# Performance work log

Measured on AMD Instinct MI355X. Metric: run time of the kernel, lower is better.

The kernel has to match this reference:

```python
import jax, jax.numpy as jnp
import numpy as np

N = 50000   # nodes
E = 800000  # directed edges
IN = 128
H = 128


def setup_inputs() -> dict:
    key = jax.random.key(0)
    k1, k2, k3, k4 = jax.random.split(key, 4)
    x = jax.random.normal(k1, (N, IN), jnp.float32)
    edge_index = jax.random.randint(k2, (2, E), 0, N, jnp.int32)
    W1 = jax.random.normal(k3, (IN, H), jnp.float32) / np.sqrt(IN)
    b1 = jnp.zeros((H,), jnp.float32)
    W2 = jax.random.normal(k4, (H, H), jnp.float32) / np.sqrt(H)
    b2 = jnp.zeros((H,), jnp.float32)
    return {"x": x, "edge_index": edge_index, "W1": W1, "b1": b1, "W2": W2, "b2": b2}


def _gcn_norm(edge_index, num_nodes):
    # PyG GCNConv default: add self-loops, symmetric normalization D^-1/2 A D^-1/2
    row, col = edge_index[0], edge_index[1]
    loop = jnp.arange(num_nodes, dtype=row.dtype)
    row = jnp.concatenate([row, loop])
    col = jnp.concatenate([col, loop])
    deg = jax.ops.segment_sum(jnp.ones_like(row, jnp.float32), row, num_segments=num_nodes)
    dinv = jnp.where(deg > 0, jax.lax.rsqrt(deg), 0.0)
    norm = dinv[row] * dinv[col]  # [E + N]
    return row, col, norm


def _gcn_conv(x, W, b, row, col, norm, num_nodes):
    xw = x @ W                                  # [N, H] dense GEMM
    msg = norm[:, None] * xw[col]               # gather + scale, [E+N, H]
    out = jax.ops.segment_sum(msg, row, num_segments=num_nodes)  # scatter-add
    return out + b


def reference(x, edge_index, W1, b1, W2, b2):
    row, col, norm = _gcn_norm(edge_index, N)
    h = _gcn_conv(x, W1, b1, row, col, norm, N)
    h = jax.nn.relu(h)
    out = _gcn_conv(h, W2, b2, row, col, norm, N)
    return out
```

## Files before the change

kernel.cpp:

```cpp
#include <hip/hip_runtime.h>

#define NN 50000
#define NE 800000
#define HD 128
#define NBK 98
#define BCAP 16384
#define FB 196
#define CVB 200

using short8 = __attribute__((ext_vector_type(8))) short;
using f32x4  = __attribute__((ext_vector_type(4))) float;

__device__ inline unsigned short rne_bf16(float v) {
    union { float f; unsigned u; } c; c.f = v;
    return (unsigned short)((c.u + 0x7fff + ((c.u >> 16) & 1)) >> 16);
}
__device__ inline float bf16_to_f32(unsigned short h) {
    union { unsigned u; float f; } c; c.u = ((unsigned)h) << 16;
    return c.f;
}


__global__ __launch_bounds__(256) void k_fill1(const int* __restrict__ ei,
                                               int* __restrict__ bcur,
                                               int2* __restrict__ pairs,
                                               const float* __restrict__ W1,
                                               const float* __restrict__ W2,
                                               unsigned short* __restrict__ hi1,
                                               unsigned short* __restrict__ lo1,
                                               unsigned short* __restrict__ hi2,
                                               unsigned short* __restrict__ lo2,
                                               const float* __restrict__ x,
                                               unsigned short* __restrict__ xb) {
    int t = threadIdx.x, b = blockIdx.x;
    if (b >= FB + 16) {
        int bb = b - (FB + 16);
        const int total = NN * HD / 8;
        for (int i = bb * 256 + t; i < total; i += CVB * 256) {
            float4 a0 = ((const float4*)x)[i * 2];
            float4 a1 = ((const float4*)x)[i * 2 + 1];
            short8 r;
            r[0] = (short)rne_bf16(a0.x); r[1] = (short)rne_bf16(a0.y);
            r[2] = (short)rne_bf16(a0.z); r[3] = (short)rne_bf16(a0.w);
            r[4] = (short)rne_bf16(a1.x); r[5] = (short)rne_bf16(a1.y);
            r[6] = (short)rne_bf16(a1.z); r[7] = (short)rne_bf16(a1.w);
            *(short8*)(xb + (size_t)i * 8) = r;
        }
        return;
    }
    if (b >= FB) {
        int bb = b - FB;
        const float* W = (bb < 8) ? W1 : W2;
        unsigned short* hi = (bb < 8) ? hi1 : hi2;
        unsigned short* lo = (bb < 8) ? lo1 : lo2;
        int tid = (bb & 7) * 256 + t;
        int lane = tid & 63;
        int ks = (tid >> 6) & 3;
        int nt = tid >> 8;
        int n = nt * 16 + (lane & 15);
        int k0 = ks * 32 + (lane >> 4) * 8;
#pragma unroll
        for (int j = 0; j < 8; ++j) {
            float v = W[(k0 + j) * HD + n];
            unsigned short h = rne_bf16(v);
            float rem = v - bf16_to_f32(h);
            hi[(size_t)tid * 8 + j] = h;
            lo[(size_t)tid * 8 + j] = rne_bf16(rem);
        }
        return;
    }
    __shared__ int dr[4096], sc[4096];
    __shared__ int hist[NBK], base[NBK];
    for (int i = t; i < NBK; i += 256) hist[i] = 0;
    __syncthreads();
    int e0 = b * 4096;
#pragma unroll
    for (int u = 0; u < 16; ++u) {
        int idx = u * 256 + t, e = e0 + idx;
        int r = -1, c = 0;
        if (e < NE) {
            r = ei[e];
            c = ei[NE + e];
            atomicAdd(&hist[r >> 9], 1);
        }
        dr[idx] = r;
        sc[idx] = c;
    }
    __syncthreads();
    for (int i = t; i < NBK; i += 256) {
        base[i] = atomicAdd(&bcur[i], hist[i]);
        hist[i] = 0;
    }
    __syncthreads();
#pragma unroll
    for (int u = 0; u < 16; ++u) {
        int idx = u * 256 + t;
        int r = dr[idx];
        if (r >= 0) {
            int bk = r >> 9;
            int pos = atomicAdd(&hist[bk], 1);
            pairs[(size_t)bk * BCAP + base[bk] + pos] = make_int2(r, sc[idx]);
        }
    }
}


__global__ __launch_bounds__(256) void k_fill2(const int2* __restrict__ pairs,
                                               const int* __restrict__ bcur,
                                               int* __restrict__ deg,
                                               int* __restrict__ offs,
                                               float* __restrict__ dinv,
                                               int* __restrict__ csr) {
    __shared__ int spart[256];
    __shared__ int cnt[512];
    __shared__ int lcur[512];
    int b = blockIdx.x, t = threadIdx.x;
    int n0 = b * 512;
    int nodes = min(512, NN - n0);

    int v = (t < NBK && t < b) ? bcur[t] : 0;
    spart[t] = v;
    __syncthreads();
#pragma unroll
    for (int o = 128; o > 0; o >>= 1) {
        if (t < o) spart[t] += spart[t + o];
        __syncthreads();
    }
    int base = spart[0];
    int tot = bcur[b];

    for (int i = t; i < 512; i += 256) cnt[i] = 0;
    __syncthreads();
    const int2* pp = pairs + (size_t)b * BCAP;
    for (int p = t; p < tot; p += 256) atomicAdd(&cnt[pp[p].x - n0], 1);
    __syncthreads();

    int d0 = (2 * t < nodes) ? cnt[2 * t] : 0;
    int d1 = (2 * t + 1 < nodes) ? cnt[2 * t + 1] : 0;
    spart[t] = d0 + d1;
    __syncthreads();
#pragma unroll
    for (int o = 1; o < 256; o <<= 1) {
        int x = (t >= o) ? spart[t - o] : 0;
        __syncthreads();
        spart[t] += x;
        __syncthreads();
    }
    int excl = spart[t] - (d0 + d1);
    int o0 = base + excl, o1 = o0 + d0;
    if (2 * t < nodes) {
        offs[n0 + 2 * t] = o0;
        lcur[2 * t] = o0;
        deg[n0 + 2 * t] = d0;
        dinv[n0 + 2 * t] = rsqrtf((float)(d0 + 1));
    }
    if (2 * t + 1 < nodes) {
        offs[n0 + 2 * t + 1] = o1;
        lcur[2 * t + 1] = o1;
        deg[n0 + 2 * t + 1] = d1;
        dinv[n0 + 2 * t + 1] = rsqrtf((float)(d1 + 1));
    }
    __syncthreads();

    for (int p = t; p < tot; p += 256) {
        int2 pr = pp[p];
        int slot = atomicAdd(&lcur[pr.x - n0], 1);
        csr[slot] = pr.y;
    }
}


__global__ __launch_bounds__(256) void k_agg_bf16(const unsigned short* __restrict__ src,
                                                  const int* __restrict__ csr,
                                                  const int* __restrict__ offs,
                                                  const int* __restrict__ deg,
                                                  const float* __restrict__ dinv,
                                                  unsigned short* __restrict__ dst) {
    int node = blockIdx.x * 4 + (threadIdx.x >> 6);
    int lane = threadIdx.x & 63;
    int q = lane >> 4;
    int sub = lane & 15;
    int o = offs[node];
    int dg = deg[node];
    float d = dinv[node];

    float acc[8];
    if (q == 0) {
        float s = d * d;
        short8 v = *(const short8*)(src + (size_t)node * HD + sub * 8);
#pragma unroll
        for (int i = 0; i < 8; ++i) acc[i] = s * bf16_to_f32((unsigned short)v[i]);
    } else {
#pragma unroll
        for (int i = 0; i < 8; ++i) acc[i] = 0.0f;
    }

    for (int base = 0; base < dg; base += 64) {
        int n = min(64, dg - base);
        int myc = (lane < n) ? csr[o + base + lane] : node;
        float myw = (lane < n) ? d * dinv[myc] : 0.0f;
        for (int j = 0; j * 4 < n; ++j) {
            int c = __shfl(myc, j * 4 + q);
            float w = __shfl(myw, j * 4 + q);
            short8 v = *(const short8*)(src + (size_t)c * HD + sub * 8);
#pragma unroll
            for (int i = 0; i < 8; ++i)
                acc[i] = fmaf(w, bf16_to_f32((unsigned short)v[i]), acc[i]);
        }
    }

#pragma unroll
    for (int i = 0; i < 8; ++i) {
        acc[i] += __shfl_xor(acc[i], 16);
        acc[i] += __shfl_xor(acc[i], 32);
    }
    if (q == 0) {
        short8 r;
#pragma unroll
        for (int i = 0; i < 8; ++i) r[i] = (short)rne_bf16(acc[i]);
        *(short8*)(dst + (size_t)node * HD + sub * 8) = r;
    }
}


template <bool RELU, bool OUTBF16>
__global__ __launch_bounds__(256) void k_gemm_mfma(const unsigned short* __restrict__ A,
                                                   const unsigned short* __restrict__ Whi,
                                                   const unsigned short* __restrict__ Wlo,
                                                   const float* __restrict__ bias,
                                                   void* __restrict__ Cout, int nrows) {
    int l = threadIdx.x & 63;
    int w = threadIdx.x >> 6;
    int row0 = blockIdx.x * 64 + w * 16;
    int arow = row0 + (l & 15);
    int kj = (l >> 4) * 8;
    bool avalid = (arow < nrows);
    const unsigned short* ap = A + (size_t)(avalid ? arow : 0) * HD + kj;

    f32x4 acc[8];
#pragma unroll
    for (int nt = 0; nt < 8; ++nt) acc[nt] = (f32x4){0.f, 0.f, 0.f, 0.f};

#pragma unroll
    for (int ks = 0; ks < 4; ++ks) {
        short8 ahi = {0, 0, 0, 0, 0, 0, 0, 0};
        if (avalid) ahi = *(const short8*)(ap + ks * 32);
#pragma unroll
        for (int nt = 0; nt < 8; ++nt) {
            size_t fo = ((size_t)(nt * 4 + ks) * 64 + l) * 8;
            short8 bhi = *(const short8*)(Whi + fo);
            short8 blo = *(const short8*)(Wlo + fo);
            acc[nt] = __builtin_amdgcn_mfma_f32_16x16x32_bf16(ahi, bhi, acc[nt], 0, 0, 0);
            acc[nt] = __builtin_amdgcn_mfma_f32_16x16x32_bf16(ahi, blo, acc[nt], 0, 0, 0);
        }
    }

#pragma unroll
    for (int nt = 0; nt < 8; ++nt) {
        int col = nt * 16 + (l & 15);
        float bv = bias[col];
#pragma unroll
        for (int r = 0; r < 4; ++r) {
            int gr = row0 + (l >> 4) * 4 + r;
            if (gr >= nrows) continue;
            float v = acc[nt][r] + bv;
            if (RELU) v = fmaxf(v, 0.f);
            if (OUTBF16)
                ((unsigned short*)Cout)[(size_t)gr * HD + col] = rne_bf16(v);
            else
                ((float*)Cout)[(size_t)gr * HD + col] = v;
        }
    }
}


extern "C" void kernel_launch(void* const* d_in, const int* in_sizes, int n_in,
                              void* d_out, int out_size, void* d_ws, size_t ws_size,
                              hipStream_t stream) {
    const float* x  = (const float*)d_in[0];
    const int*   ei = (const int*)d_in[1];
    const float* W1 = (const float*)d_in[2];
    const float* b1 = (const float*)d_in[3];
    const float* W2 = (const float*)d_in[4];
    const float* b2 = (const float*)d_in[5];
    float* out = (float*)d_out;

    char* ws = (char*)d_ws;
    size_t off = 0;
    auto alloc = [&](size_t bytes) {
        void* p = ws + off;
        off = (off + bytes + 255) & ~(size_t)255;
        return p;
    };
    int*   bcur = (int*)alloc(NBK * 4);
    int*   deg  = (int*)alloc(NN * 4);
    int*   offs = (int*)alloc(NN * 4);
    float* dinv = (float*)alloc(NN * 4);
    int*   csr  = (int*)alloc((size_t)NE * 4);
    unsigned short* xb  = (unsigned short*)alloc((size_t)NN * HD * 2);
    unsigned short* t1b = (unsigned short*)alloc((size_t)NN * HD * 2);
    char* region = (char*)alloc((size_t)NBK * BCAP * 8);
    int2* pairs = (int2*)region;
    unsigned short* hb = (unsigned short*)region;
    unsigned short* Whi1 = (unsigned short*)alloc(16384 * 2);
    unsigned short* Wlo1 = (unsigned short*)alloc(16384 * 2);
    unsigned short* Whi2 = (unsigned short*)alloc(16384 * 2);
    unsigned short* Wlo2 = (unsigned short*)alloc(16384 * 2);

    hipMemsetAsync(bcur, 0, NBK * 4, stream);
    k_fill1<<<FB + 16 + CVB, 256, 0, stream>>>(ei, bcur, pairs, W1, W2,
                                               Whi1, Wlo1, Whi2, Wlo2, x, xb);
    k_fill2<<<NBK, 256, 0, stream>>>(pairs, bcur, deg, offs, dinv, csr);

    k_agg_bf16<<<NN / 4, 256, 0, stream>>>(xb, csr, offs, deg, dinv, t1b);
    k_gemm_mfma<true, true><<<(NN + 63) / 64, 256, 0, stream>>>(t1b, Whi1, Wlo1, b1, hb, NN);

    k_agg_bf16<<<NN / 4, 256, 0, stream>>>(hb, csr, offs, deg, dinv, t1b);
    k_gemm_mfma<false, false><<<(NN + 63) / 64, 256, 0, stream>>>(t1b, Whi2, Wlo2, b2, out, NN);
}
```

Measured before the change: 216.8 us.

## Fuse neighbor aggregation with MFMA GEMM through swizzled LDS tile

Replaces the separate aggregation and GEMM kernels with one fused kernel per layer. Each block aggregates 16 nodes, four per wave, writes the bf16 rows into an XOR-swizzled shared-memory tile, then runs the 16x128 MFMA product, with each wave covering two column tiles. This drops the intermediate aggregated buffer's global write and read and halves the number of launches. In exchange each wave now processes four nodes one after another, and the grid has fewer blocks.

```diff
diff --git a/kernel.cpp b/kernel.cpp
--- a/kernel.cpp
+++ b/kernel.cpp
@@ -170,100 +170,97 @@
 }
 
 
-__global__ __launch_bounds__(256) void k_agg_bf16(const unsigned short* __restrict__ src,
+template <bool RELU, bool OUTBF16>
+__global__ __launch_bounds__(256) void k_agg_gemm(const unsigned short* __restrict__ src,
                                                   const int* __restrict__ csr,
                                                   const int* __restrict__ offs,
                                                   const int* __restrict__ deg,
                                                   const float* __restrict__ dinv,
-                                                  unsigned short* __restrict__ dst) {
-    int node = blockIdx.x * 4 + (threadIdx.x >> 6);
-    int lane = threadIdx.x & 63;
-    int q = lane >> 4;
-    int sub = lane & 15;
-    int o = offs[node];
-    int dg = deg[node];
-    float d = dinv[node];
-
-    float acc[8];
-    if (q == 0) {
-        float s = d * d;
-        short8 v = *(const short8*)(src + (size_t)node * HD + sub * 8);
-#pragma unroll
-        for (int i = 0; i < 8; ++i) acc[i] = s * bf16_to_f32((unsigned short)v[i]);
-    } else {
-#pragma unroll
-        for (int i = 0; i < 8; ++i) acc[i] = 0.0f;
-    }
-
-    for (int base = 0; base < dg; base += 64) {
-        int n = min(64, dg - base);
-        int myc = (lane < n) ? csr[o + base + lane] : node;
-        float myw = (lane < n) ? d * dinv[myc] : 0.0f;
-        for (int j = 0; j * 4 < n; ++j) {
-            int c = __shfl(myc, j * 4 + q);
-            float w = __shfl(myw, j * 4 + q);
-            short8 v = *(const short8*)(src + (size_t)c * HD + sub * 8);
-#pragma unroll
-            for (int i = 0; i < 8; ++i)
-                acc[i] = fmaf(w, bf16_to_f32((unsigned short)v[i]), acc[i]);
-        }
-    }
-
-#pragma unroll
-    for (int i = 0; i < 8; ++i) {
-        acc[i] += __shfl_xor(acc[i], 16);
-        acc[i] += __shfl_xor(acc[i], 32);
-    }
-    if (q == 0) {
-        short8 r;
-#pragma unroll
-        for (int i = 0; i < 8; ++i) r[i] = (short)rne_bf16(acc[i]);
-        *(short8*)(dst + (size_t)node * HD + sub * 8) = r;
-    }
-}
-
-
-template <bool RELU, bool OUTBF16>
-__global__ __launch_bounds__(256) void k_gemm_mfma(const unsigned short* __restrict__ A,
-                                                   const unsigned short* __restrict__ Whi,
-                                                   const unsigned short* __restrict__ Wlo,
-                                                   const float* __restrict__ bias,
-                                                   void* __restrict__ Cout, int nrows) {
-    int l = threadIdx.x & 63;
-    int w = threadIdx.x >> 6;
-    int row0 = blockIdx.x * 64 + w * 16;
-    int arow = row0 + (l & 15);
-    int kj = (l >> 4) * 8;
-    bool avalid = (arow < nrows);
-    const unsigned short* ap = A + (size_t)(avalid ? arow : 0) * HD + kj;
-
-    f32x4 acc[8];
-#pragma unroll
-    for (int nt = 0; nt < 8; ++nt) acc[nt] = (f32x4){0.f, 0.f, 0.f, 0.f};
-
+                                                  const unsigned short* __restrict__ Whi,
+                                                  const unsigned short* __restrict__ Wlo,
+                                                  const float* __restrict__ bias,
+                                                  void* __restrict__ Cout) {
+    __shared__ unsigned short As[16 * 128];
+    int t = threadIdx.x;
+    int w = t >> 6, l = t & 63;
+    int q = l >> 4, sub = l & 15;
+    int n0 = blockIdx.x * 16;
+
+#pragma unroll
+    for (int i = 0; i < 4; ++i) {
+        int row = w * 4 + i;
+        int node = n0 + row;
+        int o = offs[node];
+        int dg = deg[node];
+        float d = dinv[node];
+
+        float acc[8];
+        if (q == 0) {
+            float s = d * d;
+            short8 v = *(const short8*)(src + (size_t)node * HD + sub * 8);
+#pragma unroll
+            for (int k = 0; k < 8; ++k) acc[k] = s * bf16_to_f32((unsigned short)v[k]);
+        } else {
+#pragma unroll
+            for (int k = 0; k < 8; ++k) acc[k] = 0.0f;
+        }
+
+        for (int base = 0; base < dg; base += 64) {
+            int n = min(64, dg - base);
+            int myc = (l < n) ? csr[o + base + l] : node;
+            float myw = (l < n) ? d * dinv[myc] : 0.0f;
+            for (int j = 0; j * 4 < n; ++j) {
+                int c = __shfl(myc, j * 4 + q);
+                float wg = __shfl(myw, j * 4 + q);
+                short8 v = *(const short8*)(src + (size_t)c * HD + sub * 8);
+#pragma unroll
+                for (int k = 0; k < 8; ++k)
+                    acc[k] = fmaf(wg, bf16_to_f32((unsigned short)v[k]), acc[k]);
+            }
+        }
+#pragma unroll
+        for (int k = 0; k < 8; ++k) {
+            acc[k] += __shfl_xor(acc[k], 16);
+            acc[k] += __shfl_xor(acc[k], 32);
+        }
+        if (q == 0) {
+            short8 r;
+#pragma unroll
+            for (int k = 0; k < 8; ++k) r[k] = (short)rne_bf16(acc[k]);
+            int byte = (sub * 16) ^ ((row & 7) << 4);
+            *(short8*)((char*)As + row * 256 + byte) = r;
+        }
+    }
+    __syncthreads();
+
+    f32x4 cacc[2];
+    cacc[0] = (f32x4){0.f, 0.f, 0.f, 0.f};
+    cacc[1] = (f32x4){0.f, 0.f, 0.f, 0.f};
+    int arow = l & 15;
 #pragma unroll
     for (int ks = 0; ks < 4; ++ks) {
-        short8 ahi = {0, 0, 0, 0, 0, 0, 0, 0};
-        if (avalid) ahi = *(const short8*)(ap + ks * 32);
-#pragma unroll
-        for (int nt = 0; nt < 8; ++nt) {
+        int byte = (ks * 64 + (l >> 4) * 16) ^ ((arow & 7) << 4);
+        short8 ahi = *(const short8*)((char*)As + arow * 256 + byte);
+#pragma unroll
+        for (int i = 0; i < 2; ++i) {
+            int nt = w * 2 + i;
             size_t fo = ((size_t)(nt * 4 + ks) * 64 + l) * 8;
             short8 bhi = *(const short8*)(Whi + fo);
             short8 blo = *(const short8*)(Wlo + fo);
-            acc[nt] = __builtin_amdgcn_mfma_f32_16x16x32_bf16(ahi, bhi, acc[nt], 0, 0, 0);
-            acc[nt] = __builtin_amdgcn_mfma_f32_16x16x32_bf16(ahi, blo, acc[nt], 0, 0, 0);
-        }
-    }
-
-#pragma unroll
-    for (int nt = 0; nt < 8; ++nt) {
+            cacc[i] = __builtin_amdgcn_mfma_f32_16x16x32_bf16(ahi, bhi, cacc[i], 0, 0, 0);
+            cacc[i] = __builtin_amdgcn_mfma_f32_16x16x32_bf16(ahi, blo, cacc[i], 0, 0, 0);
+        }
+    }
+
+#pragma unroll
+    for (int i = 0; i < 2; ++i) {
+        int nt = w * 2 + i;
         int col = nt * 16 + (l & 15);
         float bv = bias[col];
 #pragma unroll
         for (int r = 0; r < 4; ++r) {
-            int gr = row0 + (l >> 4) * 4 + r;
-            if (gr >= nrows) continue;
-            float v = acc[nt][r] + bv;
+            int gr = n0 + (l >> 4) * 4 + r;
+            float v = cacc[i][r] + bv;
             if (RELU) v = fmaxf(v, 0.f);
             if (OUTBF16)
                 ((unsigned short*)Cout)[(size_t)gr * HD + col] = rne_bf16(v);
@@ -297,8 +294,7 @@
     int*   offs = (int*)alloc(NN * 4);
     float* dinv = (float*)alloc(NN * 4);
     int*   csr  = (int*)alloc((size_t)NE * 4);
-    unsigned short* xb  = (unsigned short*)alloc((size_t)NN * HD * 2);
-    unsigned short* t1b = (unsigned short*)alloc((size_t)NN * HD * 2);
+    unsigned short* xb = (unsigned short*)alloc((size_t)NN * HD * 2);
     char* region = (char*)alloc((size_t)NBK * BCAP * 8);
     int2* pairs = (int2*)region;
     unsigned short* hb = (unsigned short*)region;
@@ -312,9 +308,8 @@
                                                Whi1, Wlo1, Whi2, Wlo2, x, xb);
     k_fill2<<<NBK, 256, 0, stream>>>(pairs, bcur, deg, offs, dinv, csr);
 
-    k_agg_bf16<<<NN / 4, 256, 0, stream>>>(xb, csr, offs, deg, dinv, t1b);
-    k_gemm_mfma<true, true><<<(NN + 63) / 64, 256, 0, stream>>>(t1b, Whi1, Wlo1, b1, hb, NN);
-
-    k_agg_bf16<<<NN / 4, 256, 0, stream>>>(hb, csr, offs, deg, dinv, t1b);
-    k_gemm_mfma<false, false><<<(NN + 63) / 64, 256, 0, stream>>>(t1b, Whi2, Wlo2, b2, out, NN);
-}
+    k_agg_gemm<true, true><<<NN / 16, 256, 0, stream>>>(xb, csr, offs, deg, dinv,
+                                                        Whi1, Wlo1, b1, hb);
+    k_agg_gemm<false, false><<<NN / 16, 256, 0, stream>>>(hb, csr, offs, deg, dinv,
+                                                          Whi2, Wlo2, b2, out);
+}
```

Result: faster. 201.0 us (-7.3%).
